# Kernel tuning notes

Measured on AMD Instinct MI355X. Metric: run time of the kernel, lower is better.

## Reference

```python
import jax, jax.numpy as jnp
import numpy as np

NUM_HEADS = 4
NUM_GROUPS = 32
EPS = 1e-5


def setup_inputs() -> dict:
    key = jax.random.key(0)
    ks = jax.random.split(key, 5)
    c = 256
    x = jax.random.normal(ks[0], (2, c, 64, 64), dtype=jnp.float32)
    gn_w = jnp.ones((c,), dtype=jnp.float32)
    gn_b = jnp.zeros((c,), dtype=jnp.float32)
    qkv_w = jax.random.normal(ks[1], (3 * c, c), dtype=jnp.float32) * 0.02
    qkv_b = jax.random.normal(ks[2], (3 * c,), dtype=jnp.float32) * 0.02
    proj_w = jax.random.normal(ks[3], (c, c), dtype=jnp.float32) * 0.02
    proj_b = jnp.zeros((c,), dtype=jnp.float32)
    return {"x": x, "gn_w": gn_w, "gn_b": gn_b, "qkv_w": qkv_w,
            "qkv_b": qkv_b, "proj_w": proj_w, "proj_b": proj_b}


def reference(x, gn_w, gn_b, qkv_w, qkv_b, proj_w, proj_b):
    b, c, H, W = x.shape
    T = H * W
    xf = x.reshape(b, c, T)

    # GroupNorm(32, c): stats over (channels-in-group, T)
    xg = xf.reshape(b, NUM_GROUPS, c // NUM_GROUPS, T)
    mu = jnp.mean(xg, axis=(2, 3), keepdims=True)
    var = jnp.var(xg, axis=(2, 3), keepdims=True)
    xn = ((xg - mu) * jax.lax.rsqrt(var + EPS)).reshape(b, c, T)
    xn = xn * gn_w[None, :, None] + gn_b[None, :, None]

    # 1x1 conv1d == channel matmul: [3c, c] @ [b, c, T]
    qkv = jnp.einsum('oc,bct->bot', qkv_w, xn) + qkv_b[None, :, None]

    nh = NUM_HEADS
    ch = c // nh
    # reshape exactly as torch: (b, 3c, T) -> (b*nh, 3c//nh, T), split along dim 1
    qkv = qkv.reshape(b * nh, 3 * ch, T)
    q, k, v = jnp.split(qkv, 3, axis=1)

    scale = 1.0 / ch ** 0.25
    w = jnp.einsum('bct,bcs->bts', q * scale, k * scale)  # [b*nh, T, T]
    w = jax.nn.softmax(w, axis=-1)
    h = jnp.einsum('bts,bcs->bct', w, v)  # [b*nh, ch, T]

    h = h.reshape(b, c, T)
    h = jnp.einsum('oc,bct->bot', proj_w, h) + proj_b[None, :, None]
    return (xf + h).reshape(b, c, H, W)
```

## Files before the change

### kernel.cpp

```cpp
#include <hip/hip_runtime.h>
#include <hip/hip_bf16.h>

typedef float  f32x4  __attribute__((ext_vector_type(4)));
typedef float  f32x16 __attribute__((ext_vector_type(16)));
typedef short  s16x8  __attribute__((ext_vector_type(8)));
typedef __bf16 b16x8  __attribute__((ext_vector_type(8)));
typedef unsigned int u32x4 __attribute__((ext_vector_type(4)));

#define DI static __device__ __forceinline__

constexpr int BATCH = 2;
constexpr int C     = 256;
constexpr int T     = 4096;
constexpr int NG    = 32;
constexpr int CPG   = 8;
constexpr int NH    = 4;
constexpr int CH    = 64;

constexpr size_t STATS_OFF = 0;
constexpr size_t QKVW_OFF  = 4096;
constexpr size_t PROJW_OFF = QKVW_OFF + 393216;
constexpr size_t XNT_OFF   = PROJW_OFF + 131072;
constexpr size_t Q_OFF     = XNT_OFF + 4194304;
constexpr size_t K_OFF     = Q_OFF + 4194304;
constexpr size_t V_OFF     = K_OFF + 4194304;
constexpr size_t H_OFF     = V_OFF + 4194304;

template <typename V>
DI auto mfma_try(V a, V b, f32x4 c, int)
    -> decltype(__builtin_amdgcn_mfma_f32_16x16x32_bf16(a, b, c, 0, 0, 0)) {
  return __builtin_amdgcn_mfma_f32_16x16x32_bf16(a, b, c, 0, 0, 0);
}
template <typename V>
DI f32x4 mfma_try(V a, V b, f32x4 c, long) {
  return __builtin_amdgcn_mfma_f32_16x16x32_bf16(
      __builtin_bit_cast(b16x8, a), __builtin_bit_cast(b16x8, b), c, 0, 0, 0);
}
DI f32x4 MFMA(s16x8 a, s16x8 b, f32x4 c) { return mfma_try(a, b, c, 0); }

template <typename V>
DI auto mfma32_try(V a, V b, f32x16 c, int)
    -> decltype(__builtin_amdgcn_mfma_f32_32x32x16_bf16(a, b, c, 0, 0, 0)) {
  return __builtin_amdgcn_mfma_f32_32x32x16_bf16(a, b, c, 0, 0, 0);
}
template <typename V>
DI f32x16 mfma32_try(V a, V b, f32x16 c, long) {
  return __builtin_amdgcn_mfma_f32_32x32x16_bf16(
      __builtin_bit_cast(b16x8, a), __builtin_bit_cast(b16x8, b), c, 0, 0, 0);
}
DI f32x16 MFMA32(s16x8 a, s16x8 b, f32x16 c) { return mfma32_try(a, b, c, 0); }

DI unsigned short f2b(float f) {
  return __builtin_bit_cast(unsigned short, __float2bfloat16(f));
}
DI s16x8 ld8(const unsigned short* p) { return *(const s16x8*)p; }

DI float exp2f_(float x) {
#if __has_builtin(__builtin_amdgcn_exp2f)
  return __builtin_amdgcn_exp2f(x);
#else
  return exp2f(x);
#endif
}

DI unsigned cvtpk(float lo, float hi) {
  unsigned r;
  asm("v_cvt_pk_bf16_f32 %0, %1, %2" : "=v"(r) : "v"(lo), "v"(hi));
  return r;
}

DI void swap32(unsigned& a, unsigned& b) {
#if __has_builtin(__builtin_amdgcn_permlane32_swap)
  auto r = __builtin_amdgcn_permlane32_swap((int)a, (int)b, false, false);
  a = (unsigned)r[0];
  b = (unsigned)r[1];
#else
  unsigned as = (unsigned)__shfl_xor((int)a, 32);
  unsigned bs = (unsigned)__shfl_xor((int)b, 32);
  if (threadIdx.x & 32) a = bs; else b = as;
#endif
}

DI void stage16(const void* g, void* l) {
  __builtin_amdgcn_global_load_lds((__attribute__((address_space(1))) const void*)g,
                                   (__attribute__((address_space(3))) void*)l, 16, 0, 0);
}

DI float vsum16(f32x16 v) {
  float p0 = (v[0] + v[1]) + (v[2] + v[3]);
  float p1 = (v[4] + v[5]) + (v[6] + v[7]);
  float p2 = (v[8] + v[9]) + (v[10] + v[11]);
  float p3 = (v[12] + v[13]) + (v[14] + v[15]);
  return (p0 + p1) + (p2 + p3);
}

constexpr float SC2 = 0.18033688011f;

__global__ __launch_bounds__(256) void k_prep(const float* __restrict__ x,
                                              float2* __restrict__ part,
                                              const float* __restrict__ qkvw,
                                              const float* __restrict__ projw,
                                              uint2* __restrict__ qwb,
                                              uint2* __restrict__ pwb) {
  int blk = blockIdx.x;
  if (blk < 256) {
    const float4* base = (const float4*)(x + (size_t)blk * 8192);
    float s = 0.f, ss = 0.f;
    for (int i = threadIdx.x; i < 2048; i += 256) {
      float4 v = base[i];
      s  += v.x + v.y + v.z + v.w;
      ss += v.x * v.x + v.y * v.y + v.z * v.z + v.w * v.w;
    }
#pragma unroll
    for (int off = 32; off > 0; off >>= 1) {
      s  += __shfl_down(s, off);
      ss += __shfl_down(ss, off);
    }
    __shared__ float sm[4], sm2[4];
    int wid = threadIdx.x >> 6;
    if ((threadIdx.x & 63) == 0) { sm[wid] = s; sm2[wid] = ss; }
    __syncthreads();
    if (threadIdx.x == 0)
      part[blk] = make_float2(sm[0] + sm[1] + sm[2] + sm[3], sm2[0] + sm2[1] + sm2[2] + sm2[3]);
  } else {
    int i = (blk - 256) * 256 + threadIdx.x;
    if (i < 3 * C * C / 4) {
      float4 v = ((const float4*)qkvw)[i];
      qwb[i] = make_uint2(cvtpk(v.x, v.y), cvtpk(v.z, v.w));
    }
    if (i < C * C / 4) {
      float4 v = ((const float4*)projw)[i];
      pwb[i] = make_uint2(cvtpk(v.x, v.y), cvtpk(v.z, v.w));
    }
  }
}

__global__ __launch_bounds__(256) void k_gnapply(const float* __restrict__ x,
                                                 const float2* __restrict__ part,
                                                 const float* __restrict__ gnw,
                                                 const float* __restrict__ gnb,
                                                 unsigned short* __restrict__ xnT) {
  __shared__ float tile[64][69];
  int b = blockIdx.z, c0 = blockIdx.y * 64, t0 = blockIdx.x * 64;
  int tid = threadIdx.x;
  int tl = tid & 63, cq = tid >> 6;
  const float inv = 1.f / (float)(CPG * T);
#pragma unroll
  for (int i = 0; i < 16; i++) {
    int c = c0 + cq + i * 4;
    int g4 = (b * NG + c / CPG) * 4;
    float2 p0 = part[g4], p1 = part[g4 + 1], p2 = part[g4 + 2], p3 = part[g4 + 3];
    float S = p0.x + p1.x + p2.x + p3.x;
    float SS = p0.y + p1.y + p2.y + p3.y;
    float mu = S * inv;
    float rsd = rsqrtf(SS * inv - mu * mu + 1e-5f);
    float v = x[((size_t)b * C + c) * T + t0 + tl];
    tile[cq + i * 4][tl] = (v - mu) * rsd * gnw[c] + gnb[c];
  }
  __syncthreads();
  int unit = tid & 7, tw = tid >> 3;
#pragma unroll
  for (int it = 0; it < 2; it++) {
    int t_l = tw + it * 32;
    float v[8];
#pragma unroll
    for (int k = 0; k < 8; k++) v[k] = tile[unit * 8 + k][t_l];
    u32x4 o = {cvtpk(v[0], v[1]), cvtpk(v[2], v[3]), cvtpk(v[4], v[5]), cvtpk(v[6], v[7])};
    *(u32x4*)(xnT + ((size_t)b * T + t0 + t_l) * C + c0 + unit * 8) = o;
  }
}

__global__ __launch_bounds__(512) void k_qkv(const unsigned short* __restrict__ wq,
                                             const float* __restrict__ bias,
                                             const unsigned short* __restrict__ xnT,
                                             unsigned short* __restrict__ qb,
                                             unsigned short* __restrict__ kb,
                                             unsigned short* __restrict__ vb) {
  int b = blockIdx.z;
  int o0 = blockIdx.y * 128;
  int t0 = blockIdx.x * 128;
  int tid = threadIdx.x, lane = tid & 63, wid = tid >> 6;
  int l31 = lane & 31, h = lane >> 5;
  int ow = (wid & 3) * 32;
  int th = (wid >> 2) * 64;
  const unsigned short* xp = xnT + (size_t)b * T * C;

  __shared__ __align__(16) char smem[131072];
  unsigned short* XL = (unsigned short*)smem;
  unsigned short* WL = (unsigned short*)(smem + 65536);

#pragma unroll
  for (int call = 0; call < 8; call++) {
    int row = call * 16 + wid * 2 + h;
    stage16(xp + (size_t)(t0 + row) * C + ((l31 ^ (row & 31)) * 8),
            smem + call * 8192 + wid * 1024);
  }
#pragma unroll
  for (int call = 0; call < 8; call++) {
    int row = call * 16 + wid * 2 + h;
    stage16(wq + (size_t)(o0 + row) * C + ((l31 ^ (row & 31)) * 8),
            smem + 65536 + call * 8192 + wid * 1024);
  }
  __syncthreads();

  f32x16 acc[2] = {};
  int ro = ow + l31;
  int rosw = ro & 31;
  int rt0 = th + l31, rt1 = th + 32 + l31;
  int rt0sw = rt0 & 31, rt1sw = rt1 & 31;
#pragma unroll
  for (int kc = 0; kc < C; kc += 16) {
    int u = (kc >> 3) + h;
    s16x8 a = ld8(WL + ro * 256 + ((u ^ rosw) * 8));
    s16x8 b0 = ld8(XL + rt0 * 256 + ((u ^ rt0sw) * 8));
    s16x8 b1 = ld8(XL + rt1 * 256 + ((u ^ rt1sw) * 8));
    acc[0] = MFMA32(a, b0, acc[0]);
    acc[1] = MFMA32(a, b1, acc[1]);
  }

  int mo = o0 + ow;
  int region = (mo >> 6) % 3;
  int hh = mo / 192;
  int bh = b * NH + hh;
  int rb = mo - hh * 192 - region * 64;
  float qsc = (region == 0) ? SC2 : 1.0f;
#pragma unroll
  for (int sub = 0; sub < 2; sub++) {
    int t = t0 + th + sub * 32 + l31;
#pragma unroll
    for (int rq = 0; rq < 4; rq++) {
      int obase = mo + 4 * h + 8 * rq;
      if (region < 2) {
        unsigned short pk[4];
#pragma unroll
        for (int j = 0; j < 4; j++)
          pk[j] = f2b((acc[sub][rq * 4 + j] + bias[obase + j]) * qsc);
        unsigned short* dst = (region == 0 ? qb : kb) + ((size_t)bh * T + t) * CH + rb + 4 * h + 8 * rq;
        *(ushort4*)dst = make_ushort4(pk[0], pk[1], pk[2], pk[3]);
      } else {
#pragma unroll
        for (int j = 0; j < 4; j++)
          vb[((size_t)bh * CH + rb + 4 * h + 8 * rq + j) * T + t] =
              f2b(acc[sub][rq * 4 + j] + bias[obase + j]);
      }
    }
  }
}

__global__ __launch_bounds__(512, 2) void k_attn6(const unsigned short* __restrict__ qb,
                                                  const unsigned short* __restrict__ kb,
                                                  const unsigned short* __restrict__ vb,
                                                  unsigned short* __restrict__ hb) {
  int bid = blockIdx.x;
  int lin = (bid & 7) * 32 + (bid >> 3);
  int qt = lin & 31;
  int bh = lin >> 5;
  int tid = threadIdx.x;
  int wid = tid >> 6, lane = tid & 63;
  int l31 = lane & 31, h = lane >> 5;
  int wq = wid & 1, g = wid >> 1;
  int qbase = qt * 128 + wq * 64;

  constexpr int SG = T / 4;
  constexpr int NT = SG / 64;

  const unsigned short* qp = qb + (size_t)bh * T * CH;
  const unsigned short* kp = kb + (size_t)bh * T * CH;
  const unsigned short* vp = vb + (size_t)bh * CH * T;
  unsigned short* hp = hb + (size_t)bh * T * CH;

  __shared__ __align__(16) char smem[131072];
  char* gbase = smem + g * 32768;

  s16x8 qfA[4], qfB[4];
#pragma unroll
  for (int kc = 0; kc < 4; kc++) {
    qfA[kc] = ld8(qp + (size_t)(qbase + l31) * CH + kc * 16 + h * 8);
    qfB[kc] = ld8(qp + (size_t)(qbase + 32 + l31) * CH + kc * 16 + h * 8);
  }

  f32x16 O0a = {}, O1a = {}, O0b = {}, O1b = {};
  float lA = 0.f, lB = 0.f;

  int srow = lane >> 3, su = lane & 7;
  const unsigned short* kS = kp + (size_t)(g * SG + srow) * CH + (su ^ srow) * 8;
  const unsigned short* vS = vp + (size_t)srow * T + g * SG + (su ^ srow) * 8;

#define STAGE(BUF, TT)                                                        \
  {                                                                           \
    char* slab_ = gbase + (BUF) * 16384;                                      \
    if (wq == 0) {                                                            \
      const unsigned short* s_ = kS + (size_t)(TT) * 64 * CH;                 \
      _Pragma("unroll") for (int j_ = 0; j_ < 8; j_++)                        \
          stage16(s_ + j_ * 8 * CH, slab_ + j_ * 1024);                       \
    } else {                                                                  \
      const unsigned short* s_ = vS + (size_t)(TT) * 64;                      \
      _Pragma("unroll") for (int j_ = 0; j_ < 8; j_++)                        \
          stage16(s_ + (size_t)j_ * 8 * T, slab_ + 8192 + j_ * 1024);         \
    }                                                                         \
  }

  int buf = 0;
  STAGE(0, 0);
  __syncthreads();

  int rsw = l31 & 7;
  int row0 = l31, row1 = 32 + l31;
  for (int t = 0; t < NT; ++t) {
    if (t + 1 < NT) STAGE(buf ^ 1, t + 1);
    const unsigned short* Kt = (const unsigned short*)(gbase + buf * 16384);
    const unsigned short* Vt = Kt + 4096;

    f32x16 S0a = {}, S1a = {}, S0b = {}, S1b = {};
    __builtin_amdgcn_s_setprio(1);
#pragma unroll
    for (int kc = 0; kc < 4; kc++) {
      s16x8 k0 = ld8(Kt + row0 * 64 + (((kc * 2 + h) ^ rsw) * 8));
      s16x8 k1 = ld8(Kt + row1 * 64 + (((kc * 2 + h) ^ rsw) * 8));
      S0a = MFMA32(k0, qfA[kc], S0a);
      S0b = MFMA32(k0, qfB[kc], S0b);
      S1a = MFMA32(k1, qfA[kc], S1a);
      S1b = MFMA32(k1, qfB[kc], S1b);
    }
    __builtin_amdgcn_s_setprio(0);

#pragma unroll
    for (int j = 0; j < 16; j++) {
      S0a[j] = exp2f_(S0a[j]);
      S1a[j] = exp2f_(S1a[j]);
      S0b[j] = exp2f_(S0b[j]);
      S1b[j] = exp2f_(S1b[j]);
    }
    lA += vsum16(S0a) + vsum16(S1a);
    lB += vsum16(S0b) + vsum16(S1b);

    __builtin_amdgcn_s_setprio(1);
#pragma unroll
    for (int sch = 0; sch < 4; sch++) {
      const f32x16& Sa = (sch < 2) ? S0a : S1a;
      const f32x16& Sb = (sch < 2) ? S0b : S1b;
      int o = (sch & 1) * 8;
      unsigned a0 = cvtpk(Sa[o + 0], Sa[o + 1]), a1 = cvtpk(Sa[o + 2], Sa[o + 3]);
      unsigned a2 = cvtpk(Sa[o + 4], Sa[o + 5]), a3 = cvtpk(Sa[o + 6], Sa[o + 7]);
      swap32(a0, a2); swap32(a1, a3);
      u32x4 pA = {a0, a1, a2, a3};
      unsigned b0 = cvtpk(Sb[o + 0], Sb[o + 1]), b1 = cvtpk(Sb[o + 2], Sb[o + 3]);
      unsigned b2 = cvtpk(Sb[o + 4], Sb[o + 5]), b3 = cvtpk(Sb[o + 6], Sb[o + 7]);
      swap32(b0, b2); swap32(b1, b3);
      u32x4 pB = {b0, b1, b2, b3};
      s16x8 pfA = __builtin_bit_cast(s16x8, pA);
      s16x8 pfB = __builtin_bit_cast(s16x8, pB);
      s16x8 v0 = ld8(Vt + row0 * 64 + (((sch * 2 + h) ^ rsw) * 8));
      s16x8 v1 = ld8(Vt + row1 * 64 + (((sch * 2 + h) ^ rsw) * 8));
      O0a = MFMA32(v0, pfA, O0a);
      O1a = MFMA32(v1, pfA, O1a);
      O0b = MFMA32(v0, pfB, O0b);
      O1b = MFMA32(v1, pfB, O1b);
    }
    __builtin_amdgcn_s_setprio(0);
    __syncthreads();
    buf ^= 1;
  }

  lA += __shfl_xor(lA, 32);
  lB += __shfl_xor(lB, 32);
  constexpr int SLOT = 67;
  float* cmbA = (float*)smem;
  float* cmbB = cmbA + 256 * SLOT;
  if (g >= 2) {
    float* dst = cmbA + (((g - 2) * 2 + wq) * 64 + lane) * SLOT;
#pragma unroll
    for (int j = 0; j < 16; j++) {
      dst[j] = O0a[j]; dst[16 + j] = O1a[j];
      dst[32 + j] = O0b[j]; dst[48 + j] = O1b[j];
    }
    dst[64] = lA; dst[65] = lB;
  }
  __syncthreads();
  if (g < 2) {
    const float* src = cmbA + ((g * 2 + wq) * 64 + lane) * SLOT;
#pragma unroll
    for (int j = 0; j < 16; j++) {
      O0a[j] += src[j];
      O1a[j] += src[16 + j];
      O0b[j] += src[32 + j];
      O1b[j] += src[48 + j];
    }
    lA += src[64]; lB += src[65];
  }
  __syncthreads();
  if (g == 1) {
    float* dst = cmbB + (wq * 64 + lane) * SLOT;
#pragma unroll
    for (int j = 0; j < 16; j++) {
      dst[j] = O0a[j]; dst[16 + j] = O1a[j];
      dst[32 + j] = O0b[j]; dst[48 + j] = O1b[j];
    }
    dst[64] = lA; dst[65] = lB;
  }
  __syncthreads();
  if (g == 0) {
    const float* src = cmbB + (wq * 64 + lane) * SLOT;
    float invA = 1.f / (lA + src[64]);
    float invB = 1.f / (lB + src[65]);
    int qA = qbase + l31, qB = qbase + 32 + l31;
#pragma unroll
    for (int j = 0; j < 16; j += 2) {
      int ch = (j & 3) + 8 * (j >> 2) + 4 * h;
      float y0 = (O0a[j] + src[j]) * invA;
      float y1 = (O0a[j + 1] + src[j + 1]) * invA;
      *(unsigned*)(hp + (size_t)qA * CH + ch) = cvtpk(y0, y1);
      float z0 = (O1a[j] + src[16 + j]) * invA;
      float z1 = (O1a[j + 1] + src[16 + j + 1]) * invA;
      *(unsigned*)(hp + (size_t)qA * CH + 32 + ch) = cvtpk(z0, z1);
      float u0 = (O0b[j] + src[32 + j]) * invB;
      float u1 = (O0b[j + 1] + src[32 + j + 1]) * invB;
      *(unsigned*)(hp + (size_t)qB * CH + ch) = cvtpk(u0, u1);
      float w0 = (O1b[j] + src[48 + j]) * invB;
      float w1 = (O1b[j + 1] + src[48 + j + 1]) * invB;
      *(unsigned*)(hp + (size_t)qB * CH + 32 + ch) = cvtpk(w0, w1);
    }
  }
}

__global__ __launch_bounds__(256) void k_proj(const unsigned short* __restrict__ wp,
                                              const float* __restrict__ bias,
                                              const unsigned short* __restrict__ hb,
                                              const float* __restrict__ x,
                                              float* __restrict__ out) {
  int b = blockIdx.z, t0 = blockIdx.x * 32;
  int lane = threadIdx.x & 63, wid = threadIdx.x >> 6;
  int l31 = lane & 31, h = lane >> 5;
  int ow = wid * 64;
  f32x16 acc0 = {}, acc1 = {};
#pragma unroll
  for (int kc = 0; kc < C; kc += 16) {
    int head = kc >> 6;
    int coff = (kc & 63) + h * 8;
    s16x8 bf = ld8(hb + ((size_t)(b * NH + head) * T + t0 + l31) * CH + coff);
    s16x8 a0 = ld8(wp + (size_t)(ow + l31) * C + kc + h * 8);
    s16x8 a1 = ld8(wp + (size_t)(ow + 32 + l31) * C + kc + h * 8);
    acc0 = MFMA32(a0, bf, acc0);
    acc1 = MFMA32(a1, bf, acc1);
  }
  int t = t0 + l31;
#pragma unroll
  for (int chunk = 0; chunk < 2; chunk++) {
    const f32x16& acc = chunk ? acc1 : acc0;
#pragma unroll
    for (int reg = 0; reg < 16; reg++) {
      int o = ow + chunk * 32 + (reg & 3) + 8 * (reg >> 2) + 4 * h;
      size_t idx = ((size_t)b * C + o) * T + t;
      out[idx] = x[idx] + bias[o] + acc[reg];
    }
  }
}

extern "C" void kernel_launch(void* const* d_in, const int* in_sizes, int n_in,
                              void* d_out, int out_size, void* d_ws, size_t ws_size,
                              hipStream_t stream) {
  const float* x     = (const float*)d_in[0];
  const float* gnw   = (const float*)d_in[1];
  const float* gnb   = (const float*)d_in[2];
  const float* qkvw  = (const float*)d_in[3];
  const float* qkvb  = (const float*)d_in[4];
  const float* projw = (const float*)d_in[5];
  const float* projb = (const float*)d_in[6];
  float* out = (float*)d_out;
  char* ws = (char*)d_ws;

  float2* part          = (float2*)(ws + STATS_OFF);
  unsigned short* qw_b  = (unsigned short*)(ws + QKVW_OFF);
  unsigned short* pw_b  = (unsigned short*)(ws + PROJW_OFF);
  unsigned short* xnT   = (unsigned short*)(ws + XNT_OFF);
  unsigned short* qbuf  = (unsigned short*)(ws + Q_OFF);
  unsigned short* kbuf  = (unsigned short*)(ws + K_OFF);
  unsigned short* vbuf  = (unsigned short*)(ws + V_OFF);
  unsigned short* hbuf  = (unsigned short*)(ws + H_OFF);

  k_prep   <<<dim3(448), dim3(256), 0, stream>>>(x, part, qkvw, projw, (uint2*)qw_b, (uint2*)pw_b);
  k_gnapply<<<dim3(T / 64, C / 64, BATCH), dim3(256), 0, stream>>>(x, part, gnw, gnb, xnT);
  k_qkv    <<<dim3(T / 128, (3 * C) / 128, BATCH), dim3(512), 0, stream>>>(qw_b, qkvb, xnT, qbuf, kbuf, vbuf);
  k_attn6  <<<dim3(256), dim3(512), 0, stream>>>(qbuf, kbuf, vbuf, hbuf);
  k_proj   <<<dim3(T / 32, 1, BATCH), dim3(256), 0, stream>>>(pw_b, projb, hbuf, x, out);
}
```

Before: 85.39 us.

## Stage projection weights and head outputs in swizzled LDS tiles for k_proj

The output-projection kernel now copies a 128-row weight tile and a 64-token head-output tile into shared memory with an XOR swizzle. The MFMA loop then reads operands from LDS instead of issuing strided global loads. The grid is retiled to 64 tokens by 128 output channels per block. The goal is better operand reuse and coalesced loads, at the cost of 96KB of LDS per block, which limits occupancy, and a single sync with no overlap between load and compute.

```diff
diff --git a/kernel.cpp b/kernel.cpp
--- a/kernel.cpp
+++ b/kernel.cpp
@@ -428,28 +428,53 @@
                                               const unsigned short* __restrict__ hb,
                                               const float* __restrict__ x,
                                               float* __restrict__ out) {
-  int b = blockIdx.z, t0 = blockIdx.x * 32;
-  int lane = threadIdx.x & 63, wid = threadIdx.x >> 6;
+  int b = blockIdx.z, o0 = blockIdx.y * 128, t0 = blockIdx.x * 64;
+  int tid = threadIdx.x, lane = tid & 63, wid = tid >> 6;
   int l31 = lane & 31, h = lane >> 5;
-  int ow = wid * 64;
+  int ow = wid * 32;
+
+  __shared__ __align__(16) char smem[98304];
+  unsigned short* WL = (unsigned short*)smem;
+  unsigned short* HL = (unsigned short*)(smem + 65536);
+
+#pragma unroll
+  for (int call = 0; call < 16; call++) {
+    int rbase = call * 8 + wid * 2;
+    int row = rbase + h;
+    stage16(wp + (size_t)(o0 + row) * C + ((l31 ^ (row & 31)) * 8),
+            smem + rbase * 512);
+  }
+#pragma unroll
+  for (int call = 0; call < 8; call++) {
+    int rbase = call * 8 + wid * 2;
+    int row = rbase + h;
+    int du = l31 ^ (row & 31);
+    stage16(hb + ((size_t)(b * NH + (du >> 3)) * T + t0 + row) * CH + (du & 7) * 8,
+            smem + 65536 + rbase * 512);
+  }
+  __syncthreads();
+
   f32x16 acc0 = {}, acc1 = {};
+  int ro = ow + l31, rosw = ro & 31;
+  int rt0 = l31, rt1 = 32 + l31;
+  int rt0sw = rt0 & 31, rt1sw = rt1 & 31;
 #pragma unroll
   for (int kc = 0; kc < C; kc += 16) {
-    int head = kc >> 6;
-    int coff = (kc & 63) + h * 8;
-    s16x8 bf = ld8(hb + ((size_t)(b * NH + head) * T + t0 + l31) * CH + coff);
-    s16x8 a0 = ld8(wp + (size_t)(ow + l31) * C + kc + h * 8);
-    s16x8 a1 = ld8(wp + (size_t)(ow + 32 + l31) * C + kc + h * 8);
-    acc0 = MFMA32(a0, bf, acc0);
-    acc1 = MFMA32(a1, bf, acc1);
-  }
-  int t = t0 + l31;
-#pragma unroll
-  for (int chunk = 0; chunk < 2; chunk++) {
-    const f32x16& acc = chunk ? acc1 : acc0;
+    int u = (kc >> 3) + h;
+    s16x8 a  = ld8(WL + ro * 256 + ((u ^ rosw) * 8));
+    s16x8 b0 = ld8(HL + rt0 * 256 + ((u ^ rt0sw) * 8));
+    s16x8 b1 = ld8(HL + rt1 * 256 + ((u ^ rt1sw) * 8));
+    acc0 = MFMA32(a, b0, acc0);
+    acc1 = MFMA32(a, b1, acc1);
+  }
+
+#pragma unroll
+  for (int sub = 0; sub < 2; sub++) {
+    const f32x16& acc = sub ? acc1 : acc0;
+    int t = t0 + sub * 32 + l31;
 #pragma unroll
     for (int reg = 0; reg < 16; reg++) {
-      int o = ow + chunk * 32 + (reg & 3) + 8 * (reg >> 2) + 4 * h;
+      int o = o0 + ow + (reg & 3) + 8 * (reg >> 2) + 4 * h;
       size_t idx = ((size_t)b * C + o) * T + t;
       out[idx] = x[idx] + bias[o] + acc[reg];
     }
@@ -482,5 +507,5 @@
   k_gnapply<<<dim3(T / 64, C / 64, BATCH), dim3(256), 0, stream>>>(x, part, gnw, gnb, xnT);
   k_qkv    <<<dim3(T / 128, (3 * C) / 128, BATCH), dim3(512), 0, stream>>>(qw_b, qkvb, xnT, qbuf, kbuf, vbuf);
   k_attn6  <<<dim3(256), dim3(512), 0, stream>>>(qbuf, kbuf, vbuf, hbuf);
-  k_proj   <<<dim3(T / 32, 1, BATCH), dim3(256), 0, stream>>>(pw_b, projb, hbuf, x, out);
-}
+  k_proj   <<<dim3(T / 64, C / 128, BATCH), dim3(256), 0, stream>>>(pw_b, projb, hbuf, x, out);
+}
```

Measured after the change: 74.18 us. 13.1% less time.
